# Kernel tuning notes

Hardware: AMD Instinct MI355X
Metric: run time of the kernel (lower is better)

## Reference

```python
import jax, jax.numpy as jnp
import numpy as np

B, S, HIDDEN = 2, 2048, 2048
HEADS, GROUPS, KVC = 16, 4, 128
HPG = HEADS // GROUPS  # heads per group
LAYER_INDEX = 2
SOFTMAX_SCALE = KVC ** -0.5
ROPE_THETA = 10000.0


def _rope_tables(seq_len, dim, dtype=jnp.float32):
    inv_freq = 1.0 / (ROPE_THETA ** (jnp.arange(0, dim, 2, dtype=jnp.float32) / dim))
    t = jnp.arange(seq_len, dtype=jnp.float32)
    freqs = jnp.outer(t, inv_freq)  # [S, dim/2]
    return jnp.cos(freqs).astype(dtype), jnp.sin(freqs).astype(dtype)


def _apply_rope(x, cos, sin):
    # x: [b, s, h, d]; rotate-half (GPT-NeoX style)
    d2 = x.shape[-1] // 2
    x1, x2 = x[..., :d2], x[..., d2:]
    c = cos[None, :, None, :]
    s = sin[None, :, None, :]
    return jnp.concatenate([x1 * c - x2 * s, x2 * c + x1 * s], axis=-1)


def setup_inputs() -> dict:
    key = jax.random.key(0)
    k1, k2, k3, k4 = jax.random.split(key, 4)
    std = HIDDEN ** -0.5
    return {
        "x": jax.random.normal(k1, (B, S, HIDDEN), dtype=jnp.float32),
        "w_q": jax.random.normal(k2, (HIDDEN, HEADS * KVC), dtype=jnp.float32) * std,
        "w_kv": jax.random.normal(k3, (HIDDEN, 2 * GROUPS * KVC), dtype=jnp.float32) * std,
        "w_dense": jax.random.normal(k4, (HEADS * KVC, HIDDEN), dtype=jnp.float32) * std,
    }


def reference(x, w_q, w_kv, w_dense):
    b, s, _ = x.shape
    # QKV projections
    q = (x @ w_q).reshape(b, s, HEADS, KVC)                 # [b,s,H,d]
    kv = (x @ w_kv).reshape(b, s, 2, GROUPS, KVC)
    k, v = kv[:, :, 0], kv[:, :, 1]                          # [b,s,G,d]
    # Rotary embeddings on q and k
    cos, sin = _rope_tables(s, KVC, x.dtype)
    q = _apply_rope(q, cos, sin)
    k = _apply_rope(k, cos, sin)
    # GQA attention with per-layer scaling trick:
    # scores computed at scale/softmax of layer_index, cast fp32, rescaled back.
    qg = q.reshape(b, s, GROUPS, HPG, KVC)
    scores = jnp.einsum("bqghd,bkgd->bghqk", qg, k) * (SOFTMAX_SCALE / LAYER_INDEX)
    scores = scores.astype(jnp.float32) * LAYER_INDEX
    # causal mask
    causal = jnp.tril(jnp.ones((s, s), dtype=bool))
    mask_value = jnp.finfo(jnp.float32).min
    scores = jnp.where(causal[None, None, None, :, :], scores, mask_value)
    probs = jax.nn.softmax(scores, axis=-1).astype(x.dtype)  # dropout p=0 (eval)
    ctx = jnp.einsum("bghqk,bkgd->bqghd", probs, v).reshape(b, s, HEADS * KVC)
    return ctx @ w_dense
```

## Files before the change

### kernel.cpp

```cpp
#include <hip/hip_runtime.h>
#include <hip/hip_bf16.h>
#include <stdint.h>

typedef unsigned short u16;
typedef __bf16 bf16x8 __attribute__((ext_vector_type(8)));
typedef float f32x4 __attribute__((ext_vector_type(4)));

#define S_LEN 2048
#define BATCH 2
#define NHEADS 16
#define NGROUPS 4
#define DHEAD 128
#define QKV_W 3072

__device__ __forceinline__ float bf2f(u16 u) {
  union { uint32_t i; float f; } v; v.i = ((uint32_t)u) << 16; return v.f;
}
__device__ __forceinline__ u16 f2bf(float f) {
  union { float f; uint32_t i; } v; v.f = f;
  uint32_t r = v.i + 0x7FFF + ((v.i >> 16) & 1);
  return (u16)(r >> 16);
}
__device__ __forceinline__ void llds16(const void* g, void* l) {
  __builtin_amdgcn_global_load_lds(
      (const __attribute__((address_space(1))) uint32_t*)g,
      (__attribute__((address_space(3))) uint32_t*)l, 16, 0, 0);
}

__device__ __forceinline__ void store_out(u16* C, long i, float v) { C[i] = f2bf(v); }
__device__ __forceinline__ void store_out(float* C, long i, float v) { C[i] = v; }

__global__ void rope_tables_k(float* __restrict__ cosT, float* __restrict__ sinT) {
  int i = blockIdx.x * 256 + threadIdx.x;
  int s = i >> 6, j = i & 63;
  float inv = exp2f(-(float)j * 0.20762050593045983f);
  float ang = (float)s * inv;
  float sv, cv;
  sincosf(ang, &sv, &cv);
  cosT[i] = cv; sinT[i] = sv;
}

__global__ void cvt_f32_bf16(const float* __restrict__ in, u16* __restrict__ out) {
  long i = ((long)blockIdx.x * 256 + threadIdx.x) * 4;
  float4 v = *(const float4*)(in + i);
  ushort4 o;
  o.x = f2bf(v.x); o.y = f2bf(v.y); o.z = f2bf(v.z); o.w = f2bf(v.w);
  *(ushort4*)(out + i) = o;
}

__global__ void transpose_f32_bf16(const float* __restrict__ in, u16* __restrict__ out,
                                   int R, int C) {
  __shared__ u16 tile[32][33];
  int c0 = blockIdx.x * 32, r0 = blockIdx.y * 32;
  int tx = threadIdx.x, ty = threadIdx.y;
  for (int i = 0; i < 32; i += 8)
    tile[ty + i][tx] = f2bf(in[(long)(r0 + ty + i) * C + c0 + tx]);
  __syncthreads();
  for (int i = 0; i < 32; i += 8)
    out[(long)(c0 + ty + i) * R + r0 + tx] = tile[tx][ty + i];
}

template <typename OutT>
__global__ __launch_bounds__(256) void gemm_bt(
    const u16* __restrict__ A, const u16* __restrict__ Bt, OutT* __restrict__ C,
    int M, int N, int K) {
  __shared__ __align__(16) __bf16 As[128 * 32];
  __shared__ __align__(16) __bf16 Bs[128 * 32];
  const int tid = threadIdx.x;
  const int wv = tid >> 6;
  const int lane = tid & 63;
  const int quad = lane >> 4;
  const int l16 = lane & 15;
  const int bm = blockIdx.y * 128;
  const int bn = blockIdx.x * 128;

  f32x4 acc[4][4] = {};

  const int arow = wv * 32 + (lane >> 2);
  const int kseg = (lane & 3) * 8;
  const int wm = (wv >> 1) * 64, wn = (wv & 1) * 64;

  for (int k0 = 0; k0 < K; k0 += 32) {
    __syncthreads();
    const u16* ga0 = A + (long)(bm + arow) * K + k0 + kseg;
    llds16(ga0, &As[arow * 32 + kseg]);
    llds16(ga0 + (long)16 * K, &As[(arow + 16) * 32 + kseg]);
    const u16* gb0 = Bt + (long)(bn + arow) * K + k0 + kseg;
    llds16(gb0, &Bs[arow * 32 + kseg]);
    llds16(gb0 + (long)16 * K, &Bs[(arow + 16) * 32 + kseg]);
    __syncthreads();

    bf16x8 af[4], bfr[4];
#pragma unroll
    for (int mt = 0; mt < 4; ++mt)
      af[mt] = *(const bf16x8*)&As[(wm + mt * 16 + l16) * 32 + quad * 8];
#pragma unroll
    for (int nt = 0; nt < 4; ++nt)
      bfr[nt] = *(const bf16x8*)&Bs[(wn + nt * 16 + l16) * 32 + quad * 8];
#pragma unroll
    for (int mt = 0; mt < 4; ++mt)
#pragma unroll
      for (int nt = 0; nt < 4; ++nt)
        acc[mt][nt] = __builtin_amdgcn_mfma_f32_16x16x32_bf16(
            af[mt], bfr[nt], acc[mt][nt], 0, 0, 0);
  }

#pragma unroll
  for (int mt = 0; mt < 4; ++mt)
#pragma unroll
    for (int nt = 0; nt < 4; ++nt)
#pragma unroll
      for (int r = 0; r < 4; ++r) {
        int row = bm + wm + mt * 16 + quad * 4 + r;
        int col = bn + wn + nt * 16 + l16;
        store_out(C, (long)row * N + col, acc[mt][nt][r]);
      }
}

__global__ void rope_q_k(u16* __restrict__ qkv, const float* __restrict__ cosT,
                         const float* __restrict__ sinT) {
  long i = (long)blockIdx.x * 256 + threadIdx.x;
  int j = i & 63;
  long rest = i >> 6;
  int h = rest & 15;
  long bs = rest >> 4;
  int s = bs & (S_LEN - 1);
  long base = bs * QKV_W + h * DHEAD + j;
  float x1 = bf2f(qkv[base]), x2 = bf2f(qkv[base + 64]);
  float c = cosT[s * 64 + j], sn = sinT[s * 64 + j];
  qkv[base] = f2bf(x1 * c - x2 * sn);
  qkv[base + 64] = f2bf(x2 * c + x1 * sn);
}

__global__ void rope_k_k(const u16* __restrict__ qkv, u16* __restrict__ Kb,
                         const float* __restrict__ cosT, const float* __restrict__ sinT) {
  long i = (long)blockIdx.x * 256 + threadIdx.x;
  int j = i & 63;
  long rest = i >> 6;
  int g = rest & 3;
  long bs = rest >> 2;
  int s = bs & (S_LEN - 1);
  int b = (int)(bs >> 11);
  long src = bs * QKV_W + 2048 + g * 128 + j;
  float x1 = bf2f(qkv[src]), x2 = bf2f(qkv[src + 64]);
  float c = cosT[s * 64 + j], sn = sinT[s * 64 + j];
  long dst = ((long)(b * NGROUPS + g) * S_LEN + s) * DHEAD + j;
  Kb[dst] = f2bf(x1 * c - x2 * sn);
  Kb[dst + 64] = f2bf(x2 * c + x1 * sn);
}

__global__ void v_trans_k(const u16* __restrict__ qkv, u16* __restrict__ Vt) {
  __shared__ u16 tile[32][33];
  int s0 = blockIdx.x * 32, d0 = blockIdx.y * 32;
  int bg = blockIdx.z;
  int b = bg >> 2, g = bg & 3;
  int tx = threadIdx.x, ty = threadIdx.y;
  for (int i = 0; i < 32; i += 8) {
    long s = s0 + ty + i;
    tile[ty + i][tx] = qkv[((long)b * S_LEN + s) * QKV_W + 2560 + g * 128 + d0 + tx];
  }
  __syncthreads();
  for (int i = 0; i < 32; i += 8) {
    int d = d0 + ty + i;
    Vt[((long)(b * NGROUPS + g) * DHEAD + d) * S_LEN + s0 + tx] = tile[tx][ty + i];
  }
}

__global__ __launch_bounds__(256, 2) void attn_k5(
    const u16* __restrict__ Q,
    const u16* __restrict__ Kb,
    const u16* __restrict__ Vt,
    u16* __restrict__ ctx) {
  __shared__ __align__(16) __bf16 Ks[2][64 * 128];
  __shared__ __align__(16) __bf16 Vts[2][128 * 64];
  __shared__ __align__(16) __bf16 Ps[64 * 64];

  const int h = blockIdx.y, b = blockIdx.z, g = h >> 2;
  const int tid = threadIdx.x, wv = tid >> 6, lane = tid & 63;
  const int quad = lane >> 4, l16 = lane & 15;
  const float SCALE = 0.08838834764831845f;

  const long kbase = (long)(b * NGROUPS + g) * S_LEN * DHEAD;
  const long vbase = (long)(b * NGROUPS + g) * DHEAD * S_LEN;

  const int krow_off = lane >> 4;
  const int vrow_off = lane >> 3;

  const __bf16 oneb = (__bf16)((l16 == 0) ? 1.0f : 0.0f);
  const bf16x8 bones = {oneb, oneb, oneb, oneb, oneb, oneb, oneb, oneb};

  for (int pass = 0; pass < 2; ++pass) {
    const int tile = pass == 0 ? (int)blockIdx.x : 31 - (int)blockIdx.x;
    const int q0 = tile * 64;
    const int nch = tile + 1;

    bf16x8 aq[4];
    {
      const u16* qp = Q + (long)(b * S_LEN + q0 + wv * 16 + l16) * QKV_W + h * DHEAD + quad * 8;
#pragma unroll
      for (int ds = 0; ds < 4; ++ds)
        aq[ds] = *(const bf16x8*)(qp + ds * 32);
    }

#pragma unroll
    for (int i = 0; i < 4; ++i) {
      int r0 = wv * 16 + i * 4;
      int row = r0 + krow_off;
      int c = l16 ^ (row & 15);
      llds16(Kb + kbase + (long)row * DHEAD + c * 8, &Ks[0][r0 * 128 + lane * 8]);
    }
#pragma unroll
    for (int i = 0; i < 4; ++i) {
      int d0 = wv * 32 + i * 8;
      int row = d0 + vrow_off;
      int c = (lane & 7) ^ (row & 7);
      llds16(Vt + vbase + (long)row * S_LEN + c * 8, &Vts[0][d0 * 64 + lane * 8]);
    }
    __syncthreads();

    f32x4 Oacc[9] = {};

    for (int kc = 0; kc < nch; ++kc) {
      const int cur = kc & 1;
      if (kc + 1 < nch) {
        const int nxt = cur ^ 1;
#pragma unroll
        for (int i = 0; i < 4; ++i) {
          int r0 = wv * 16 + i * 4;
          int row = r0 + krow_off;
          int c = l16 ^ (row & 15);
          llds16(Kb + kbase + (long)((kc + 1) * 64 + row) * DHEAD + c * 8,
                 &Ks[nxt][r0 * 128 + lane * 8]);
        }
#pragma unroll
        for (int i = 0; i < 4; ++i) {
          int d0 = wv * 32 + i * 8;
          int row = d0 + vrow_off;
          int c = (lane & 7) ^ (row & 7);
          llds16(Vt + vbase + (long)row * S_LEN + (kc + 1) * 64 + c * 8,
                 &Vts[nxt][d0 * 64 + lane * 8]);
        }
      }

      f32x4 sacc[4] = {};
#pragma unroll
      for (int ds = 0; ds < 4; ++ds) {
        int pos0 = ((ds * 4 + quad) ^ l16) * 8;
#pragma unroll
        for (int nt = 0; nt < 4; ++nt) {
          bf16x8 bk = *(const bf16x8*)&Ks[cur][(nt * 16 + l16) * 128 + pos0];
          sacc[nt] = __builtin_amdgcn_mfma_f32_16x16x32_bf16(aq[ds], bk, sacc[nt], 0, 0, 0);
        }
      }

#pragma unroll
      for (int nt = 0; nt < 4; ++nt)
#pragma unroll
        for (int r = 0; r < 4; ++r) {
          int qrow = q0 + wv * 16 + quad * 4 + r;
          int key = kc * 64 + nt * 16 + l16;
          float p = (key <= qrow) ? __expf(sacc[nt][r] * SCALE) : 0.f;
          int qlocal = quad * 4 + r;
          int chunk = nt * 2 + (l16 >> 3);
          int pos = chunk ^ (qlocal & 7);
          Ps[(wv * 16 + qlocal) * 64 + pos * 8 + (l16 & 7)] = (__bf16)p;
        }

      bf16x8 ap[2];
#pragma unroll
      for (int kf = 0; kf < 2; ++kf) {
        int pos = ((kf * 4 + quad) ^ (l16 & 7)) * 8;
        ap[kf] = *(const bf16x8*)&Ps[(wv * 16 + l16) * 64 + pos];
      }
#pragma unroll
      for (int nt = 0; nt < 8; ++nt)
#pragma unroll
        for (int kf = 0; kf < 2; ++kf) {
          int pos = ((kf * 4 + quad) ^ (l16 & 7)) * 8;
          bf16x8 bv = *(const bf16x8*)&Vts[cur][(nt * 16 + l16) * 64 + pos];
          Oacc[nt] = __builtin_amdgcn_mfma_f32_16x16x32_bf16(ap[kf], bv, Oacc[nt], 0, 0, 0);
        }
      Oacc[8] = __builtin_amdgcn_mfma_f32_16x16x32_bf16(ap[0], bones, Oacc[8], 0, 0, 0);
      Oacc[8] = __builtin_amdgcn_mfma_f32_16x16x32_bf16(ap[1], bones, Oacc[8], 0, 0, 0);

      __syncthreads();
    }

    float lsum[4];
#pragma unroll
    for (int r = 0; r < 4; ++r)
      lsum[r] = __shfl(Oacc[8][r], quad << 4, 64);

    const long obase = ((long)(b * S_LEN + q0 + wv * 16) * NHEADS + h) * DHEAD;
#pragma unroll
    for (int nt = 0; nt < 8; ++nt)
#pragma unroll
      for (int r = 0; r < 4; ++r) {
        int lrow = quad * 4 + r;
        ctx[obase + (long)lrow * NHEADS * DHEAD + nt * 16 + l16] =
            f2bf(Oacc[nt][r] / lsum[r]);
      }
  }
}

extern "C" void kernel_launch(void* const* d_in, const int* in_sizes, int n_in,
                              void* d_out, int out_size, void* d_ws, size_t ws_size,
                              hipStream_t stream) {
  const float* x   = (const float*)d_in[0];
  const float* wq  = (const float*)d_in[1];
  const float* wkv = (const float*)d_in[2];
  const float* wd  = (const float*)d_in[3];
  float* out = (float*)d_out;

  char* ws = (char*)d_ws;
  float* cosT  = (float*)(ws + 0);
  float* sinT  = (float*)(ws + 524288);
  u16* wqkvT = (u16*)(ws + 1048576);
  u16* wdT   = (u16*)(ws + 13631488);
  u16* xb    = (u16*)(ws + 22020096);
  u16* qkv   = (u16*)(ws + 38797312);
  u16* Kb    = (u16*)(ws + 63963136);
  u16* Vt    = (u16*)(ws + 68157440);
  u16* ctx   = (u16*)(ws + 72351744);

  rope_tables_k<<<512, 256, 0, stream>>>(cosT, sinT);
  cvt_f32_bf16<<<8192, 256, 0, stream>>>(x, xb);
  transpose_f32_bf16<<<dim3(64, 64), dim3(32, 8), 0, stream>>>(wq, wqkvT, 2048, 2048);
  transpose_f32_bf16<<<dim3(32, 64), dim3(32, 8), 0, stream>>>(wkv, wqkvT + (long)2048 * 2048, 2048, 1024);
  transpose_f32_bf16<<<dim3(64, 64), dim3(32, 8), 0, stream>>>(wd, wdT, 2048, 2048);

  gemm_bt<u16><<<dim3(24, 32), 256, 0, stream>>>(xb, wqkvT, qkv, 4096, 3072, 2048);

  rope_q_k<<<16384, 256, 0, stream>>>(qkv, cosT, sinT);
  rope_k_k<<<4096, 256, 0, stream>>>(qkv, Kb, cosT, sinT);
  v_trans_k<<<dim3(64, 4, 8), dim3(32, 8), 0, stream>>>(qkv, Vt);

  attn_k5<<<dim3(16, 16, 2), 256, 0, stream>>>(qkv, Kb, Vt, ctx);

  gemm_bt<float><<<dim3(16, 32), 256, 0, stream>>>(ctx, wdT, out, 4096, 2048, 2048);
}
```

Before: 318.0 us.

## Merge prep and rope kernels, compute rope inline, shrink GEMM N-tile to 64

Merges the input conversion and three weight transposes into one launch, and merges the q-rope, k-rope and V transpose into a second launch. The sin/cos values are now computed inline, so the table kernel and its global reads go away. The GEMM tile shrinks from 128x128 to 128x64, doubling the grid, with launch bounds set to six blocks per SM. This cuts launch overhead and improves fill on the GPU at the cost of more redundant A-tile loads and extra sincos arithmetic per element.

```diff
diff --git a/kernel.cpp b/kernel.cpp
--- a/kernel.cpp
+++ b/kernel.cpp
@@ -30,29 +30,32 @@
 __device__ __forceinline__ void store_out(u16* C, long i, float v) { C[i] = f2bf(v); }
 __device__ __forceinline__ void store_out(float* C, long i, float v) { C[i] = v; }
 
-__global__ void rope_tables_k(float* __restrict__ cosT, float* __restrict__ sinT) {
-  int i = blockIdx.x * 256 + threadIdx.x;
-  int s = i >> 6, j = i & 63;
-  float inv = exp2f(-(float)j * 0.20762050593045983f);
-  float ang = (float)s * inv;
-  float sv, cv;
-  sincosf(ang, &sv, &cv);
-  cosT[i] = cv; sinT[i] = sv;
-}
-
-__global__ void cvt_f32_bf16(const float* __restrict__ in, u16* __restrict__ out) {
-  long i = ((long)blockIdx.x * 256 + threadIdx.x) * 4;
-  float4 v = *(const float4*)(in + i);
-  ushort4 o;
-  o.x = f2bf(v.x); o.y = f2bf(v.y); o.z = f2bf(v.z); o.w = f2bf(v.w);
-  *(ushort4*)(out + i) = o;
-}
-
-__global__ void transpose_f32_bf16(const float* __restrict__ in, u16* __restrict__ out,
-                                   int R, int C) {
+__global__ void prep_all(const float* __restrict__ x,
+                         const float* __restrict__ wq,
+                         const float* __restrict__ wkv,
+                         const float* __restrict__ wd,
+                         u16* __restrict__ xb,
+                         u16* __restrict__ wqkvT,
+                         u16* __restrict__ wdT) {
+  const int z = blockIdx.z;
+  if (z >= 3) {
+    long base = ((long)(z - 3) * 4096 + blockIdx.y * 64 + blockIdx.x) * 1024 +
+                threadIdx.x * 4;
+    float4 v = *(const float4*)(x + base);
+    ushort4 o;
+    o.x = f2bf(v.x); o.y = f2bf(v.y); o.z = f2bf(v.z); o.w = f2bf(v.w);
+    *(ushort4*)(xb + base) = o;
+    return;
+  }
+  const float* in; u16* out; int R, C;
+  if (z == 0)      { in = wq;  out = wqkvT;                       R = 2048; C = 2048; }
+  else if (z == 1) { if (blockIdx.x >= 32) return;
+                     in = wkv; out = wqkvT + (long)2048 * 2048;   R = 2048; C = 1024; }
+  else             { in = wd;  out = wdT;                         R = 2048; C = 2048; }
+
   __shared__ u16 tile[32][33];
+  int tx = threadIdx.x & 31, ty = threadIdx.x >> 5;
   int c0 = blockIdx.x * 32, r0 = blockIdx.y * 32;
-  int tx = threadIdx.x, ty = threadIdx.y;
   for (int i = 0; i < 32; i += 8)
     tile[ty + i][tx] = f2bf(in[(long)(r0 + ty + i) * C + c0 + tx]);
   __syncthreads();
@@ -60,47 +63,102 @@
     out[(long)(c0 + ty + i) * R + r0 + tx] = tile[tx][ty + i];
 }
 
+__global__ void prep_qkv(u16* __restrict__ qkv, u16* __restrict__ Kb,
+                         u16* __restrict__ Vt) {
+  const int bid = blockIdx.x;
+  const int tid = threadIdx.x;
+  if (bid < 16384) {
+    long i = (long)bid * 256 + tid;
+    int j = i & 63;
+    long rest = i >> 6;
+    int h = rest & 15;
+    long bs = rest >> 4;
+    int s = bs & (S_LEN - 1);
+    float inv = exp2f(-(float)j * 0.20762050593045983f);
+    float sv, cv;
+    sincosf((float)s * inv, &sv, &cv);
+    long base = bs * QKV_W + h * DHEAD + j;
+    float x1 = bf2f(qkv[base]), x2 = bf2f(qkv[base + 64]);
+    qkv[base] = f2bf(x1 * cv - x2 * sv);
+    qkv[base + 64] = f2bf(x2 * cv + x1 * sv);
+    return;
+  }
+  if (bid < 20480) {
+    long i = (long)(bid - 16384) * 256 + tid;
+    int j = i & 63;
+    long rest = i >> 6;
+    int g = rest & 3;
+    long bs = rest >> 2;
+    int s = bs & (S_LEN - 1);
+    int b = (int)(bs >> 11);
+    float inv = exp2f(-(float)j * 0.20762050593045983f);
+    float sv, cv;
+    sincosf((float)s * inv, &sv, &cv);
+    long src = bs * QKV_W + 2048 + g * 128 + j;
+    float x1 = bf2f(qkv[src]), x2 = bf2f(qkv[src + 64]);
+    long dst = ((long)(b * NGROUPS + g) * S_LEN + s) * DHEAD + j;
+    Kb[dst] = f2bf(x1 * cv - x2 * sv);
+    Kb[dst + 64] = f2bf(x2 * cv + x1 * sv);
+    return;
+  }
+  int vb = bid - 20480;
+  int sx = vb & 63, dy = (vb >> 6) & 3, bg = vb >> 8;
+  int b = bg >> 2, g = bg & 3;
+  __shared__ u16 tile[32][33];
+  int tx = tid & 31, ty = tid >> 5;
+  int s0 = sx * 32, d0 = dy * 32;
+  for (int i = 0; i < 32; i += 8) {
+    long s = s0 + ty + i;
+    tile[ty + i][tx] = qkv[((long)b * S_LEN + s) * QKV_W + 2560 + g * 128 + d0 + tx];
+  }
+  __syncthreads();
+  for (int i = 0; i < 32; i += 8) {
+    int d = d0 + ty + i;
+    Vt[((long)(b * NGROUPS + g) * DHEAD + d) * S_LEN + s0 + tx] = tile[tx][ty + i];
+  }
+}
+
 template <typename OutT>
-__global__ __launch_bounds__(256) void gemm_bt(
+__global__ __launch_bounds__(256, 6) void gemm_bt(
     const u16* __restrict__ A, const u16* __restrict__ Bt, OutT* __restrict__ C,
     int M, int N, int K) {
   __shared__ __align__(16) __bf16 As[128 * 32];
-  __shared__ __align__(16) __bf16 Bs[128 * 32];
+  __shared__ __align__(16) __bf16 Bs[64 * 32];
   const int tid = threadIdx.x;
   const int wv = tid >> 6;
   const int lane = tid & 63;
   const int quad = lane >> 4;
   const int l16 = lane & 15;
   const int bm = blockIdx.y * 128;
-  const int bn = blockIdx.x * 128;
-
-  f32x4 acc[4][4] = {};
-
-  const int arow = wv * 32 + (lane >> 2);
-  const int kseg = (lane & 3) * 8;
-  const int wm = (wv >> 1) * 64, wn = (wv & 1) * 64;
+  const int bn = blockIdx.x * 64;
+
+  f32x4 acc[4][2] = {};
+
+  const int arow = tid >> 2;
+  const int kseg = (tid & 3) * 8;
+  const int wm = (wv & 1) * 64, wn = (wv >> 1) * 32;
+
+  const u16* Ab = A + (long)(bm + arow) * K + kseg;
+  const u16* Bb = Bt + (long)(bn + arow) * K + kseg;
 
   for (int k0 = 0; k0 < K; k0 += 32) {
     __syncthreads();
-    const u16* ga0 = A + (long)(bm + arow) * K + k0 + kseg;
-    llds16(ga0, &As[arow * 32 + kseg]);
-    llds16(ga0 + (long)16 * K, &As[(arow + 16) * 32 + kseg]);
-    const u16* gb0 = Bt + (long)(bn + arow) * K + k0 + kseg;
-    llds16(gb0, &Bs[arow * 32 + kseg]);
-    llds16(gb0 + (long)16 * K, &Bs[(arow + 16) * 32 + kseg]);
+    llds16(Ab + k0, &As[arow * 32 + kseg]);
+    llds16(Ab + (long)64 * K + k0, &As[(arow + 64) * 32 + kseg]);
+    llds16(Bb + k0, &Bs[arow * 32 + kseg]);
     __syncthreads();
 
-    bf16x8 af[4], bfr[4];
+    bf16x8 af[4], bfr[2];
 #pragma unroll
     for (int mt = 0; mt < 4; ++mt)
       af[mt] = *(const bf16x8*)&As[(wm + mt * 16 + l16) * 32 + quad * 8];
 #pragma unroll
-    for (int nt = 0; nt < 4; ++nt)
+    for (int nt = 0; nt < 2; ++nt)
       bfr[nt] = *(const bf16x8*)&Bs[(wn + nt * 16 + l16) * 32 + quad * 8];
 #pragma unroll
     for (int mt = 0; mt < 4; ++mt)
 #pragma unroll
-      for (int nt = 0; nt < 4; ++nt)
+      for (int nt = 0; nt < 2; ++nt)
         acc[mt][nt] = __builtin_amdgcn_mfma_f32_16x16x32_bf16(
             af[mt], bfr[nt], acc[mt][nt], 0, 0, 0);
   }
@@ -108,62 +166,13 @@
 #pragma unroll
   for (int mt = 0; mt < 4; ++mt)
 #pragma unroll
-    for (int nt = 0; nt < 4; ++nt)
+    for (int nt = 0; nt < 2; ++nt)
 #pragma unroll
       for (int r = 0; r < 4; ++r) {
         int row = bm + wm + mt * 16 + quad * 4 + r;
         int col = bn + wn + nt * 16 + l16;
         store_out(C, (long)row * N + col, acc[mt][nt][r]);
       }
-}
-
-__global__ void rope_q_k(u16* __restrict__ qkv, const float* __restrict__ cosT,
-                         const float* __restrict__ sinT) {
-  long i = (long)blockIdx.x * 256 + threadIdx.x;
-  int j = i & 63;
-  long rest = i >> 6;
-  int h = rest & 15;
-  long bs = rest >> 4;
-  int s = bs & (S_LEN - 1);
-  long base = bs * QKV_W + h * DHEAD + j;
-  float x1 = bf2f(qkv[base]), x2 = bf2f(qkv[base + 64]);
-  float c = cosT[s * 64 + j], sn = sinT[s * 64 + j];
-  qkv[base] = f2bf(x1 * c - x2 * sn);
-  qkv[base + 64] = f2bf(x2 * c + x1 * sn);
-}
-
-__global__ void rope_k_k(const u16* __restrict__ qkv, u16* __restrict__ Kb,
-                         const float* __restrict__ cosT, const float* __restrict__ sinT) {
-  long i = (long)blockIdx.x * 256 + threadIdx.x;
-  int j = i & 63;
-  long rest = i >> 6;
-  int g = rest & 3;
-  long bs = rest >> 2;
-  int s = bs & (S_LEN - 1);
-  int b = (int)(bs >> 11);
-  long src = bs * QKV_W + 2048 + g * 128 + j;
-  float x1 = bf2f(qkv[src]), x2 = bf2f(qkv[src + 64]);
-  float c = cosT[s * 64 + j], sn = sinT[s * 64 + j];
-  long dst = ((long)(b * NGROUPS + g) * S_LEN + s) * DHEAD + j;
-  Kb[dst] = f2bf(x1 * c - x2 * sn);
-  Kb[dst + 64] = f2bf(x2 * c + x1 * sn);
-}
-
-__global__ void v_trans_k(const u16* __restrict__ qkv, u16* __restrict__ Vt) {
-  __shared__ u16 tile[32][33];
-  int s0 = blockIdx.x * 32, d0 = blockIdx.y * 32;
-  int bg = blockIdx.z;
-  int b = bg >> 2, g = bg & 3;
-  int tx = threadIdx.x, ty = threadIdx.y;
-  for (int i = 0; i < 32; i += 8) {
-    long s = s0 + ty + i;
-    tile[ty + i][tx] = qkv[((long)b * S_LEN + s) * QKV_W + 2560 + g * 128 + d0 + tx];
-  }
-  __syncthreads();
-  for (int i = 0; i < 32; i += 8) {
-    int d = d0 + ty + i;
-    Vt[((long)(b * NGROUPS + g) * DHEAD + d) * S_LEN + s0 + tx] = tile[tx][ty + i];
-  }
 }
 
 __global__ __launch_bounds__(256, 2) void attn_k5(
@@ -313,8 +322,6 @@
   float* out = (float*)d_out;
 
   char* ws = (char*)d_ws;
-  float* cosT  = (float*)(ws + 0);
-  float* sinT  = (float*)(ws + 524288);
   u16* wqkvT = (u16*)(ws + 1048576);
   u16* wdT   = (u16*)(ws + 13631488);
   u16* xb    = (u16*)(ws + 22020096);
@@ -323,19 +330,13 @@
   u16* Vt    = (u16*)(ws + 68157440);
   u16* ctx   = (u16*)(ws + 72351744);
 
-  rope_tables_k<<<512, 256, 0, stream>>>(cosT, sinT);
-  cvt_f32_bf16<<<8192, 256, 0, stream>>>(x, xb);
-  transpose_f32_bf16<<<dim3(64, 64), dim3(32, 8), 0, stream>>>(wq, wqkvT, 2048, 2048);
-  transpose_f32_bf16<<<dim3(32, 64), dim3(32, 8), 0, stream>>>(wkv, wqkvT + (long)2048 * 2048, 2048, 1024);
-  transpose_f32_bf16<<<dim3(64, 64), dim3(32, 8), 0, stream>>>(wd, wdT, 2048, 2048);
-
-  gemm_bt<u16><<<dim3(24, 32), 256, 0, stream>>>(xb, wqkvT, qkv, 4096, 3072, 2048);
-
-  rope_q_k<<<16384, 256, 0, stream>>>(qkv, cosT, sinT);
-  rope_k_k<<<4096, 256, 0, stream>>>(qkv, Kb, cosT, sinT);
-  v_trans_k<<<dim3(64, 4, 8), dim3(32, 8), 0, stream>>>(qkv, Vt);
+  prep_all<<<dim3(64, 64, 5), 256, 0, stream>>>(x, wq, wkv, wd, xb, wqkvT, wdT);
+
+  gemm_bt<u16><<<dim3(48, 32), 256, 0, stream>>>(xb, wqkvT, qkv, 4096, 3072, 2048);
+
+  prep_qkv<<<22528, 256, 0, stream>>>(qkv, Kb, Vt);
 
   attn_k5<<<dim3(16, 16, 2), 256, 0, stream>>>(qkv, Kb, Vt, ctx);
 
-  gemm_bt<float><<<dim3(16, 32), 256, 0, stream>>>(ctx, wdT, out, 4096, 2048, 2048);
-}
+  gemm_bt<float><<<dim3(32, 32), 256, 0, stream>>>(ctx, wdT, out, 4096, 2048, 2048);
+}
```

After: 337.9 us. 1.06x slower.
